# Kernel tuning notes

Hardware: AMD Instinct MI355X
Metric: run time of the kernel (lower is better)

## Reference

```python
import jax, jax.numpy as jnp
import numpy as np

N_IN, N_HID, N_OUT = 128, 1024, 64
B, T = 128, 256
SIGMA_NEU = 0.05
ALPHA = 0.25

def setup_inputs() -> dict:
    key = jax.random.key(0)
    ks = jax.random.split(key, 6)
    input_signal = jax.random.normal(ks[0], (B, T, N_IN), dtype=jnp.float32)
    hidden = jax.random.normal(ks[1], (B, N_HID), dtype=jnp.float32)
    w_in_w = jax.random.normal(ks[2], (N_HID, N_IN), dtype=jnp.float32) / np.sqrt(N_IN)
    w_hh_w = jax.random.normal(ks[3], (N_HID, N_HID), dtype=jnp.float32) / np.sqrt(N_HID)
    w_hh_b = jnp.zeros((N_HID,), dtype=jnp.float32)
    w_out_w = jax.random.normal(ks[4], (N_OUT, N_HID), dtype=jnp.float32) / np.sqrt(N_HID)
    alpha = jnp.full((N_HID,), ALPHA, dtype=jnp.float32)
    noise_raw = jax.random.normal(ks[5], (B, N_HID), dtype=jnp.float32)
    return {
        'input_signal': input_signal,
        'hidden': hidden,
        'w_in_w': w_in_w,
        'w_hh_w': w_hh_w,
        'w_hh_b': w_hh_b,
        'w_out_w': w_out_w,
        'alpha': alpha,
        'noise_raw': noise_raw,
        'perturbation_timing': 100,
    }

def reference(input_signal, hidden, w_in_w, w_hh_w, w_hh_b, w_out_w, alpha, noise_raw, perturbation_timing):
    # input_signal: [B, T, n_in] -> time-major [T, B, n_in]
    x = jnp.swapaxes(input_signal, 0, 1)
    length = x.shape[0]
    # neural noise injected only at t == perturbation_timing (torch: randn*sigma*sqrt(alpha))
    noise = noise_raw * SIGMA_NEU * jnp.sqrt(alpha)

    def step(h, inp):
        t, x_t = inp
        activated = jnp.tanh(h)
        tmp = x_t @ w_in_w.T + activated @ w_hh_w.T + w_hh_b  # [B, n_hid]
        h_new = (1.0 - alpha) * h + alpha * tmp
        h_new = jnp.where(t == perturbation_timing, h_new + noise, h_new)
        out = h_new @ w_out_w.T  # [B, n_out]
        return h_new, (h_new, out)

    h_final, (hs, outs) = jax.lax.scan(step, hidden, (jnp.arange(length), x))
    hidden_list = jnp.swapaxes(hs, 0, 1)   # [B, T, n_hid]
    output_list = jnp.swapaxes(outs, 0, 1)  # [B, T, n_out]
    return hidden_list, output_list, h_final
```

## Files before the change

kernel.cpp:

```cpp
#include <hip/hip_runtime.h>

typedef _Float16 half8 __attribute__((ext_vector_type(8)));
typedef float floatx4 __attribute__((ext_vector_type(4)));
typedef float floatx2 __attribute__((ext_vector_type(2)));

#define N_IN   128
#define N_HID  1024
#define N_OUT  64
#define BB     128
#define TT     256

#define WHH_STRIDE 1032
#define WIN_STRIDE 136
#define RED_STRIDE 33

__device__ __forceinline__ float tanh_fast(float v) {
    float e = __expf(2.0f * v);
    return 1.0f - 2.0f / (e + 1.0f);
}

__global__ __launch_bounds__(256, 1) void rnn_seq_kernel(
    const float* __restrict__ x,
    const float* __restrict__ h0,
    const float* __restrict__ w_in,
    const float* __restrict__ w_hh,
    const float* __restrict__ w_hh_b,
    const float* __restrict__ alpha,
    const float* __restrict__ noise_raw,
    const int* __restrict__ pt_ptr,
    float* __restrict__ out,
    _Float16* __restrict__ actbuf,
    unsigned int* __restrict__ flags)
{
    __shared__ _Float16 Whh_hi[32 * WHH_STRIDE];
    __shared__ _Float16 Whh_lo[32 * WHH_STRIDE];
    __shared__ _Float16 Win_hi[32 * WIN_STRIDE];
    __shared__ _Float16 Win_lo[32 * WIN_STRIDE];
    __shared__ float red[4 * 16 * RED_STRIDE];

    const int tid  = threadIdx.x;
    const int bid  = blockIdx.x;
    const int g    = bid & 7;
    const int s    = bid >> 3;
    const int w    = tid >> 6;
    const int lane = tid & 63;
    const int quad = lane >> 4;
    const int mrow = lane & 15;

    for (int p = 0; p < 32; ++p) {
        int f4 = tid + (p << 8);
        int c  = f4 >> 8;
        int k4 = (f4 & 255) << 2;
        floatx4 wv = *(const floatx4*)(w_hh + ((size_t)(s * 32 + c) << 10) + k4);
        #pragma unroll
        for (int i = 0; i < 4; ++i) {
            float v = wv[i];
            _Float16 hi = (_Float16)v;
            _Float16 lo = (_Float16)((v - (float)hi) * 1024.0f);
            Whh_hi[c * WHH_STRIDE + k4 + i] = hi;
            Whh_lo[c * WHH_STRIDE + k4 + i] = lo;
        }
    }
    for (int p = 0; p < 4; ++p) {
        int f4 = tid + (p << 8);
        int c  = f4 >> 5;
        int k4 = (f4 & 31) << 2;
        floatx4 wv = *(const floatx4*)(w_in + ((size_t)(s * 32 + c) << 7) + k4);
        #pragma unroll
        for (int i = 0; i < 4; ++i) {
            float v = wv[i];
            _Float16 hi = (_Float16)v;
            _Float16 lo = (_Float16)((v - (float)hi) * 1024.0f);
            Win_hi[c * WIN_STRIDE + k4 + i] = hi;
            Win_lo[c * WIN_STRIDE + k4 + i] = lo;
        }
    }
    __syncthreads();

    half8 bh0[8], bl0[8], bh1[8], bl1[8];
    #pragma unroll
    for (int kc = 0; kc < 8; ++kc) {
        int kb = (w << 8) + (kc << 5) + (quad << 3);
        bh0[kc] = *(const half8*)&Whh_hi[mrow * WHH_STRIDE + kb];
        bl0[kc] = *(const half8*)&Whh_lo[mrow * WHH_STRIDE + kb];
        bh1[kc] = *(const half8*)&Whh_hi[(16 + mrow) * WHH_STRIDE + kb];
        bl1[kc] = *(const half8*)&Whh_lo[(16 + mrow) * WHH_STRIDE + kb];
    }
    half8 wi_h0, wi_l0, wi_h1, wi_l1;
    {
        int kb = (w << 5) + (quad << 3);
        wi_h0 = *(const half8*)&Win_hi[mrow * WIN_STRIDE + kb];
        wi_l0 = *(const half8*)&Win_lo[mrow * WIN_STRIDE + kb];
        wi_h1 = *(const half8*)&Win_hi[(16 + mrow) * WIN_STRIDE + kb];
        wi_l1 = *(const half8*)&Win_lo[(16 + mrow) * WIN_STRIDE + kb];
    }

    const int r   = tid >> 4;
    const int c2  = tid & 15;
    const int b   = g * 16 + r;
    const int j0  = s * 32 + 2 * c2;
    const floatx2 a2  = *(const floatx2*)&alpha[j0];
    const floatx2 bi2 = *(const floatx2*)&w_hh_b[j0];
    const floatx2 nr2 = *(const floatx2*)&noise_raw[((size_t)b << 10) + j0];
    const float n0 = nr2.x * 0.05f * __builtin_sqrtf(a2.x);
    const float n1 = nr2.y * 0.05f * __builtin_sqrtf(a2.y);
    const int pt = *pt_ptr;
    floatx2 h2 = *(const floatx2*)&h0[((size_t)b << 10) + j0];
    float hA = h2.x, hB = h2.y;

    {
        unsigned int* act1_32 = (unsigned int*)(actbuf + BB * N_HID);
        union { _Float16 h[2]; unsigned int u; } pk;
        pk.h[0] = (_Float16)tanh_fast(hA);
        pk.h[1] = (_Float16)tanh_fast(hB);
        __hip_atomic_store(&act1_32[(((unsigned)b << 10) + j0) >> 1], pk.u,
                           __ATOMIC_RELAXED, __HIP_MEMORY_SCOPE_AGENT);
    }
    __syncthreads();
    if (tid == 0)
        __hip_atomic_store(&flags[((unsigned)g) * 32u + s], 1u,
                           __ATOMIC_RELAXED, __HIP_MEMORY_SCOPE_AGENT);

    float* hidden_list = out;
    float* h_final = out + (size_t)BB * TT * N_HID + (size_t)BB * TT * N_OUT;
    const int arow = g * 16 + mrow;

    for (int t = 0; t < TT; ++t) {
        {
            const unsigned tok = (unsigned)t + 1u;
            const unsigned fidx = ((unsigned)t * 8u + g) * 32u + (w << 3) + (lane & 7);
            while (true) {
                unsigned v = __hip_atomic_load(&flags[fidx], __ATOMIC_RELAXED,
                                               __HIP_MEMORY_SCOPE_AGENT);
                if (__ballot(v == tok) == ~0ull) break;
                __builtin_amdgcn_s_sleep(1);
            }
        }

        half8 afr[8];
        {
            const unsigned long long* actq = (const unsigned long long*)
                (actbuf + (size_t)((t & 1) ^ 1) * (BB * N_HID));
            const unsigned long long* p =
                actq + ((((size_t)arow << 10) + (w << 8) + (quad << 3)) >> 2);
            #pragma unroll
            for (int kc = 0; kc < 8; ++kc) {
                union { unsigned long long u[2]; half8 h; } cv;
                cv.u[0] = __hip_atomic_load(p + kc * 8,     __ATOMIC_RELAXED,
                                            __HIP_MEMORY_SCOPE_AGENT);
                cv.u[1] = __hip_atomic_load(p + kc * 8 + 1, __ATOMIC_RELAXED,
                                            __HIP_MEMORY_SCOPE_AGENT);
                afr[kc] = cv.h;
            }
        }
        half8 xfr;
        {
            const float* xp = x + (((size_t)arow << 8) + t) * N_IN + (w << 5) + (quad << 3);
            floatx4 x0 = *(const floatx4*)xp;
            floatx4 x1 = *(const floatx4*)(xp + 4);
            #pragma unroll
            for (int i = 0; i < 4; ++i) { xfr[i] = (_Float16)x0[i]; xfr[4 + i] = (_Float16)x1[i]; }
        }

        floatx4 acch0 = {0.f,0.f,0.f,0.f}, acch1 = {0.f,0.f,0.f,0.f};
        floatx4 accl0 = {0.f,0.f,0.f,0.f}, accl1 = {0.f,0.f,0.f,0.f};

        acch0 = __builtin_amdgcn_mfma_f32_16x16x32_f16(xfr, wi_h0, acch0, 0, 0, 0);
        accl0 = __builtin_amdgcn_mfma_f32_16x16x32_f16(xfr, wi_l0, accl0, 0, 0, 0);
        acch1 = __builtin_amdgcn_mfma_f32_16x16x32_f16(xfr, wi_h1, acch1, 0, 0, 0);
        accl1 = __builtin_amdgcn_mfma_f32_16x16x32_f16(xfr, wi_l1, accl1, 0, 0, 0);

        #pragma unroll
        for (int kc = 0; kc < 8; ++kc) {
            acch0 = __builtin_amdgcn_mfma_f32_16x16x32_f16(afr[kc], bh0[kc], acch0, 0, 0, 0);
            accl0 = __builtin_amdgcn_mfma_f32_16x16x32_f16(afr[kc], bl0[kc], accl0, 0, 0, 0);
            acch1 = __builtin_amdgcn_mfma_f32_16x16x32_f16(afr[kc], bh1[kc], acch1, 0, 0, 0);
            accl1 = __builtin_amdgcn_mfma_f32_16x16x32_f16(afr[kc], bl1[kc], accl1, 0, 0, 0);
        }

        #pragma unroll
        for (int rr = 0; rr < 4; ++rr) {
            red[(w * 16 + quad * 4 + rr) * RED_STRIDE + mrow]
                = acch0[rr] + accl0[rr] * (1.0f / 1024.0f);
            red[(w * 16 + quad * 4 + rr) * RED_STRIDE + 16 + mrow]
                = acch1[rr] + accl1[rr] * (1.0f / 1024.0f);
        }
        __syncthreads();

        float t0v = bi2.x, t1v = bi2.y;
        #pragma unroll
        for (int ww = 0; ww < 4; ++ww) {
            t0v += red[(ww * 16 + r) * RED_STRIDE + 2 * c2];
            t1v += red[(ww * 16 + r) * RED_STRIDE + 2 * c2 + 1];
        }
        hA = (1.0f - a2.x) * hA + a2.x * t0v;
        hB = (1.0f - a2.y) * hB + a2.y * t1v;
        if (t == pt) { hA += n0; hB += n1; }

        floatx2 hv = {hA, hB};
        *(floatx2*)&hidden_list[(((size_t)b << 8) + t) * N_HID + j0] = hv;

        {
            union { _Float16 h[2]; unsigned int u; } pk;
            pk.h[0] = (_Float16)tanh_fast(hA);
            pk.h[1] = (_Float16)tanh_fast(hB);
            unsigned int* actw32 = (unsigned int*)(actbuf + (size_t)(t & 1) * (BB * N_HID));
            __hip_atomic_store(&actw32[(((unsigned)b << 10) + j0) >> 1], pk.u,
                               __ATOMIC_RELAXED, __HIP_MEMORY_SCOPE_AGENT);
        }

        __syncthreads();
        if (tid == 0)
            __hip_atomic_store(&flags[((unsigned)(t + 1) * 8u + g) * 32u + s],
                               (unsigned)t + 2u,
                               __ATOMIC_RELAXED, __HIP_MEMORY_SCOPE_AGENT);
    }

    *(floatx2*)&h_final[((size_t)b << 10) + j0] = (floatx2){hA, hB};
}

__global__ __launch_bounds__(256) void out_gemm_kernel(
    const float* __restrict__ hl,
    const float* __restrict__ w_out,
    float* __restrict__ outp)
{
    __shared__ _Float16 Wb[64 * 264];
    const int tid  = threadIdx.x;
    const int w    = tid >> 6;
    const int lane = tid & 63;
    const int quad = lane >> 4;
    const int mrow = lane & 15;
    const size_t rowbase = (size_t)blockIdx.x << 6;

    floatx4 acc0 = {0.f,0.f,0.f,0.f}, acc1 = {0.f,0.f,0.f,0.f};
    floatx4 acc2 = {0.f,0.f,0.f,0.f}, acc3 = {0.f,0.f,0.f,0.f};

    for (int kc = 0; kc < 4; ++kc) {
        __syncthreads();
        for (int p = 0; p < 16; ++p) {
            int f4 = tid + (p << 8);
            int n  = f4 >> 6;
            int k4 = (f4 & 63) << 2;
            floatx4 wv = *(const floatx4*)(w_out + ((size_t)n << 10) + (kc << 8) + k4);
            #pragma unroll
            for (int i = 0; i < 4; ++i) Wb[n * 264 + k4 + i] = (_Float16)wv[i];
        }
        __syncthreads();
        for (int kk = 0; kk < 8; ++kk) {
            const float* ap = hl + (rowbase + (w << 4) + mrow) * 1024
                                 + (kc << 8) + (kk << 5) + (quad << 3);
            floatx4 a0v = *(const floatx4*)ap;
            floatx4 a1v = *(const floatx4*)(ap + 4);
            half8 afr;
            #pragma unroll
            for (int i = 0; i < 4; ++i) { afr[i] = (_Float16)a0v[i]; afr[4 + i] = (_Float16)a1v[i]; }
            int kb = (kk << 5) + (quad << 3);
            half8 bf0 = *(const half8*)&Wb[(mrow)      * 264 + kb];
            half8 bf1 = *(const half8*)&Wb[(16 + mrow) * 264 + kb];
            half8 bf2 = *(const half8*)&Wb[(32 + mrow) * 264 + kb];
            half8 bf3 = *(const half8*)&Wb[(48 + mrow) * 264 + kb];
            acc0 = __builtin_amdgcn_mfma_f32_16x16x32_f16(afr, bf0, acc0, 0, 0, 0);
            acc1 = __builtin_amdgcn_mfma_f32_16x16x32_f16(afr, bf1, acc1, 0, 0, 0);
            acc2 = __builtin_amdgcn_mfma_f32_16x16x32_f16(afr, bf2, acc2, 0, 0, 0);
            acc3 = __builtin_amdgcn_mfma_f32_16x16x32_f16(afr, bf3, acc3, 0, 0, 0);
        }
    }
    size_t rb = rowbase + (w << 4);
    #pragma unroll
    for (int rr = 0; rr < 4; ++rr) {
        outp[(rb + quad * 4 + rr) * 64 +      mrow] = acc0[rr];
        outp[(rb + quad * 4 + rr) * 64 + 16 + mrow] = acc1[rr];
        outp[(rb + quad * 4 + rr) * 64 + 32 + mrow] = acc2[rr];
        outp[(rb + quad * 4 + rr) * 64 + 48 + mrow] = acc3[rr];
    }
}

extern "C" void kernel_launch(void* const* d_in, const int* in_sizes, int n_in,
                              void* d_out, int out_size, void* d_ws, size_t ws_size,
                              hipStream_t stream)
{
    const float* x      = (const float*)d_in[0];
    const float* h0     = (const float*)d_in[1];
    const float* w_in   = (const float*)d_in[2];
    const float* w_hh   = (const float*)d_in[3];
    const float* w_hh_b = (const float*)d_in[4];
    const float* w_out  = (const float*)d_in[5];
    const float* alpha  = (const float*)d_in[6];
    const float* noise  = (const float*)d_in[7];
    const int*   pt     = (const int*)d_in[8];
    float* out = (float*)d_out;

    _Float16* actbuf = (_Float16*)d_ws;
    unsigned int* flags =
        (unsigned int*)((char*)d_ws + (size_t)2 * BB * N_HID * sizeof(_Float16));

    hipLaunchKernelGGL(rnn_seq_kernel, dim3(256), dim3(256), 0, stream,
                       x, h0, w_in, w_hh, w_hh_b, alpha, noise, pt, out, actbuf, flags);

    float* output_list = out + (size_t)BB * TT * N_HID;
    hipLaunchKernelGGL(out_gemm_kernel, dim3(512), dim3(256), 0, stream,
                       out, w_out, output_list);
}
```

Before: 1.203 ms.

## Fuse output projection into recurrent kernel using fp16 hidden-state exchange buffer

Drops the separate output GEMM kernel. Each block now computes its two output columns per timestep with one lagged MFMA chain over an fp16 copy of the previous hidden state. That copy is exchanged through a new double-buffered workspace alongside the tanh activations. The change also prefetches x before the flag spin-wait, removes the s_sleep from the spin loop, and moves the hidden_list store after the flag release. It adds a second global store and load of the full hidden state per step, plus a final extra wait and GEMM after the loop.

```diff
diff --git a/kernel.cpp b/kernel.cpp
--- a/kernel.cpp
+++ b/kernel.cpp
@@ -25,11 +25,13 @@
     const float* __restrict__ w_in,
     const float* __restrict__ w_hh,
     const float* __restrict__ w_hh_b,
+    const float* __restrict__ w_out,
     const float* __restrict__ alpha,
     const float* __restrict__ noise_raw,
     const int* __restrict__ pt_ptr,
     float* __restrict__ out,
     _Float16* __restrict__ actbuf,
+    _Float16* __restrict__ hbuf,
     unsigned int* __restrict__ flags)
 {
     __shared__ _Float16 Whh_hi[32 * WHH_STRIDE];
@@ -37,6 +39,7 @@
     __shared__ _Float16 Win_hi[32 * WIN_STRIDE];
     __shared__ _Float16 Win_lo[32 * WIN_STRIDE];
     __shared__ float red[4 * 16 * RED_STRIDE];
+    __shared__ float red2[4 * 16 * 2];
 
     const int tid  = threadIdx.x;
     const int bid  = blockIdx.x;
@@ -93,6 +96,24 @@
         wi_l0 = *(const half8*)&Win_lo[mrow * WIN_STRIDE + kb];
         wi_h1 = *(const half8*)&Win_hi[(16 + mrow) * WIN_STRIDE + kb];
         wi_l1 = *(const half8*)&Win_lo[(16 + mrow) * WIN_STRIDE + kb];
+    }
+
+    half8 wo[8];
+    if (mrow < 2) {
+        const float* wp = w_out + ((size_t)(s * 2 + mrow) << 10) + (w << 8) + (quad << 3);
+        #pragma unroll
+        for (int kc = 0; kc < 8; ++kc) {
+            floatx4 a0 = *(const floatx4*)(wp + (kc << 5));
+            floatx4 a1 = *(const floatx4*)(wp + (kc << 5) + 4);
+            #pragma unroll
+            for (int i = 0; i < 4; ++i) { wo[kc][i] = (_Float16)a0[i]; wo[kc][4 + i] = (_Float16)a1[i]; }
+        }
+    } else {
+        #pragma unroll
+        for (int kc = 0; kc < 8; ++kc) {
+            #pragma unroll
+            for (int i = 0; i < 8; ++i) wo[kc][i] = (_Float16)0.0f;
+        }
     }
 
     const int r   = tid >> 4;
@@ -110,11 +131,15 @@
 
     {
         unsigned int* act1_32 = (unsigned int*)(actbuf + BB * N_HID);
-        union { _Float16 h[2]; unsigned int u; } pk;
-        pk.h[0] = (_Float16)tanh_fast(hA);
-        pk.h[1] = (_Float16)tanh_fast(hB);
-        __hip_atomic_store(&act1_32[(((unsigned)b << 10) + j0) >> 1], pk.u,
-                           __ATOMIC_RELAXED, __HIP_MEMORY_SCOPE_AGENT);
+        unsigned int* h1_32   = (unsigned int*)(hbuf   + BB * N_HID);
+        union { _Float16 h[2]; unsigned int u; } pk, pk2;
+        pk.h[0]  = (_Float16)tanh_fast(hA);
+        pk.h[1]  = (_Float16)tanh_fast(hB);
+        pk2.h[0] = (_Float16)hA;
+        pk2.h[1] = (_Float16)hB;
+        const unsigned idx = (((unsigned)b << 10) + j0) >> 1;
+        __hip_atomic_store(&act1_32[idx], pk.u,  __ATOMIC_RELAXED, __HIP_MEMORY_SCOPE_AGENT);
+        __hip_atomic_store(&h1_32[idx],   pk2.u, __ATOMIC_RELAXED, __HIP_MEMORY_SCOPE_AGENT);
     }
     __syncthreads();
     if (tid == 0)
@@ -122,10 +147,15 @@
                            __ATOMIC_RELAXED, __HIP_MEMORY_SCOPE_AGENT);
 
     float* hidden_list = out;
+    float* output_list = out + (size_t)BB * TT * N_HID;
     float* h_final = out + (size_t)BB * TT * N_HID + (size_t)BB * TT * N_OUT;
     const int arow = g * 16 + mrow;
 
     for (int t = 0; t < TT; ++t) {
+        const float* xp = x + (((size_t)arow << 8) + t) * N_IN + (w << 5) + (quad << 3);
+        floatx4 xf0 = *(const floatx4*)xp;
+        floatx4 xf1 = *(const floatx4*)(xp + 4);
+
         {
             const unsigned tok = (unsigned)t + 1u;
             const unsigned fidx = ((unsigned)t * 8u + g) * 32u + (w << 3) + (lane & 7);
@@ -133,7 +163,6 @@
                 unsigned v = __hip_atomic_load(&flags[fidx], __ATOMIC_RELAXED,
                                                __HIP_MEMORY_SCOPE_AGENT);
                 if (__ballot(v == tok) == ~0ull) break;
-                __builtin_amdgcn_s_sleep(1);
             }
         }
 
@@ -153,14 +182,25 @@
                 afr[kc] = cv.h;
             }
         }
+        half8 hfr[8];
+        {
+            const unsigned long long* hq = (const unsigned long long*)
+                (hbuf + (size_t)((t & 1) ^ 1) * (BB * N_HID));
+            const unsigned long long* p =
+                hq + ((((size_t)arow << 10) + (w << 8) + (quad << 3)) >> 2);
+            #pragma unroll
+            for (int kc = 0; kc < 8; ++kc) {
+                union { unsigned long long u[2]; half8 h; } cv;
+                cv.u[0] = __hip_atomic_load(p + kc * 8,     __ATOMIC_RELAXED,
+                                            __HIP_MEMORY_SCOPE_AGENT);
+                cv.u[1] = __hip_atomic_load(p + kc * 8 + 1, __ATOMIC_RELAXED,
+                                            __HIP_MEMORY_SCOPE_AGENT);
+                hfr[kc] = cv.h;
+            }
+        }
         half8 xfr;
-        {
-            const float* xp = x + (((size_t)arow << 8) + t) * N_IN + (w << 5) + (quad << 3);
-            floatx4 x0 = *(const floatx4*)xp;
-            floatx4 x1 = *(const floatx4*)(xp + 4);
-            #pragma unroll
-            for (int i = 0; i < 4; ++i) { xfr[i] = (_Float16)x0[i]; xfr[4 + i] = (_Float16)x1[i]; }
-        }
+        #pragma unroll
+        for (int i = 0; i < 4; ++i) { xfr[i] = (_Float16)xf0[i]; xfr[4 + i] = (_Float16)xf1[i]; }
 
         floatx4 acch0 = {0.f,0.f,0.f,0.f}, acch1 = {0.f,0.f,0.f,0.f};
         floatx4 accl0 = {0.f,0.f,0.f,0.f}, accl1 = {0.f,0.f,0.f,0.f};
@@ -178,6 +218,11 @@
             accl1 = __builtin_amdgcn_mfma_f32_16x16x32_f16(afr[kc], bl1[kc], accl1, 0, 0, 0);
         }
 
+        floatx4 aco = {0.f,0.f,0.f,0.f};
+        #pragma unroll
+        for (int kc = 0; kc < 8; ++kc)
+            aco = __builtin_amdgcn_mfma_f32_16x16x32_f16(hfr[kc], wo[kc], aco, 0, 0, 0);
+
         #pragma unroll
         for (int rr = 0; rr < 4; ++rr) {
             red[(w * 16 + quad * 4 + rr) * RED_STRIDE + mrow]
@@ -185,6 +230,11 @@
             red[(w * 16 + quad * 4 + rr) * RED_STRIDE + 16 + mrow]
                 = acch1[rr] + accl1[rr] * (1.0f / 1024.0f);
         }
+        if (mrow < 2) {
+            #pragma unroll
+            for (int rr = 0; rr < 4; ++rr)
+                red2[(w * 16 + quad * 4 + rr) * 2 + mrow] = aco[rr];
+        }
         __syncthreads();
 
         float t0v = bi2.x, t1v = bi2.y;
@@ -193,20 +243,28 @@
             t0v += red[(ww * 16 + r) * RED_STRIDE + 2 * c2];
             t1v += red[(ww * 16 + r) * RED_STRIDE + 2 * c2 + 1];
         }
+        if (t > 0 && tid < 32) {
+            int rr_ = tid >> 1, oc2 = tid & 1;
+            float v = red2[(rr_) * 2 + oc2] + red2[(16 + rr_) * 2 + oc2]
+                    + red2[(32 + rr_) * 2 + oc2] + red2[(48 + rr_) * 2 + oc2];
+            output_list[((size_t)(g * 16 + rr_) * TT + (t - 1)) * 64 + s * 2 + oc2] = v;
+        }
+
         hA = (1.0f - a2.x) * hA + a2.x * t0v;
         hB = (1.0f - a2.y) * hB + a2.y * t1v;
         if (t == pt) { hA += n0; hB += n1; }
 
-        floatx2 hv = {hA, hB};
-        *(floatx2*)&hidden_list[(((size_t)b << 8) + t) * N_HID + j0] = hv;
-
         {
-            union { _Float16 h[2]; unsigned int u; } pk;
-            pk.h[0] = (_Float16)tanh_fast(hA);
-            pk.h[1] = (_Float16)tanh_fast(hB);
+            union { _Float16 h[2]; unsigned int u; } pk, pk2;
+            pk.h[0]  = (_Float16)tanh_fast(hA);
+            pk.h[1]  = (_Float16)tanh_fast(hB);
+            pk2.h[0] = (_Float16)hA;
+            pk2.h[1] = (_Float16)hB;
             unsigned int* actw32 = (unsigned int*)(actbuf + (size_t)(t & 1) * (BB * N_HID));
-            __hip_atomic_store(&actw32[(((unsigned)b << 10) + j0) >> 1], pk.u,
-                               __ATOMIC_RELAXED, __HIP_MEMORY_SCOPE_AGENT);
+            unsigned int* hw32   = (unsigned int*)(hbuf   + (size_t)(t & 1) * (BB * N_HID));
+            const unsigned idx = (((unsigned)b << 10) + j0) >> 1;
+            __hip_atomic_store(&actw32[idx], pk.u,  __ATOMIC_RELAXED, __HIP_MEMORY_SCOPE_AGENT);
+            __hip_atomic_store(&hw32[idx],   pk2.u, __ATOMIC_RELAXED, __HIP_MEMORY_SCOPE_AGENT);
         }
 
         __syncthreads();
@@ -214,64 +272,53 @@
             __hip_atomic_store(&flags[((unsigned)(t + 1) * 8u + g) * 32u + s],
                                (unsigned)t + 2u,
                                __ATOMIC_RELAXED, __HIP_MEMORY_SCOPE_AGENT);
+
+        floatx2 hv = {hA, hB};
+        *(floatx2*)&hidden_list[(((size_t)b << 8) + t) * N_HID + j0] = hv;
     }
 
     *(floatx2*)&h_final[((size_t)b << 10) + j0] = (floatx2){hA, hB};
-}
-
-__global__ __launch_bounds__(256) void out_gemm_kernel(
-    const float* __restrict__ hl,
-    const float* __restrict__ w_out,
-    float* __restrict__ outp)
-{
-    __shared__ _Float16 Wb[64 * 264];
-    const int tid  = threadIdx.x;
-    const int w    = tid >> 6;
-    const int lane = tid & 63;
-    const int quad = lane >> 4;
-    const int mrow = lane & 15;
-    const size_t rowbase = (size_t)blockIdx.x << 6;
-
-    floatx4 acc0 = {0.f,0.f,0.f,0.f}, acc1 = {0.f,0.f,0.f,0.f};
-    floatx4 acc2 = {0.f,0.f,0.f,0.f}, acc3 = {0.f,0.f,0.f,0.f};
-
-    for (int kc = 0; kc < 4; ++kc) {
+
+    {
+        const unsigned tok = (unsigned)TT + 1u;
+        const unsigned fidx = ((unsigned)TT * 8u + g) * 32u + (w << 3) + (lane & 7);
+        while (true) {
+            unsigned v = __hip_atomic_load(&flags[fidx], __ATOMIC_RELAXED,
+                                           __HIP_MEMORY_SCOPE_AGENT);
+            if (__ballot(v == tok) == ~0ull) break;
+        }
+    }
+    {
+        half8 hfr[8];
+        const unsigned long long* hq = (const unsigned long long*)
+            (hbuf + (size_t)((TT & 1) ^ 1) * (BB * N_HID));
+        const unsigned long long* p =
+            hq + ((((size_t)arow << 10) + (w << 8) + (quad << 3)) >> 2);
+        #pragma unroll
+        for (int kc = 0; kc < 8; ++kc) {
+            union { unsigned long long u[2]; half8 h; } cv;
+            cv.u[0] = __hip_atomic_load(p + kc * 8,     __ATOMIC_RELAXED,
+                                        __HIP_MEMORY_SCOPE_AGENT);
+            cv.u[1] = __hip_atomic_load(p + kc * 8 + 1, __ATOMIC_RELAXED,
+                                        __HIP_MEMORY_SCOPE_AGENT);
+            hfr[kc] = cv.h;
+        }
+        floatx4 aco = {0.f,0.f,0.f,0.f};
+        #pragma unroll
+        for (int kc = 0; kc < 8; ++kc)
+            aco = __builtin_amdgcn_mfma_f32_16x16x32_f16(hfr[kc], wo[kc], aco, 0, 0, 0);
+        if (mrow < 2) {
+            #pragma unroll
+            for (int rr = 0; rr < 4; ++rr)
+                red2[(w * 16 + quad * 4 + rr) * 2 + mrow] = aco[rr];
+        }
         __syncthreads();
-        for (int p = 0; p < 16; ++p) {
-            int f4 = tid + (p << 8);
-            int n  = f4 >> 6;
-            int k4 = (f4 & 63) << 2;
-            floatx4 wv = *(const floatx4*)(w_out + ((size_t)n << 10) + (kc << 8) + k4);
-            #pragma unroll
-            for (int i = 0; i < 4; ++i) Wb[n * 264 + k4 + i] = (_Float16)wv[i];
-        }
-        __syncthreads();
-        for (int kk = 0; kk < 8; ++kk) {
-            const float* ap = hl + (rowbase + (w << 4) + mrow) * 1024
-                                 + (kc << 8) + (kk << 5) + (quad << 3);
-            floatx4 a0v = *(const floatx4*)ap;
-            floatx4 a1v = *(const floatx4*)(ap + 4);
-            half8 afr;
-            #pragma unroll
-            for (int i = 0; i < 4; ++i) { afr[i] = (_Float16)a0v[i]; afr[4 + i] = (_Float16)a1v[i]; }
-            int kb = (kk << 5) + (quad << 3);
-            half8 bf0 = *(const half8*)&Wb[(mrow)      * 264 + kb];
-            half8 bf1 = *(const half8*)&Wb[(16 + mrow) * 264 + kb];
-            half8 bf2 = *(const half8*)&Wb[(32 + mrow) * 264 + kb];
-            half8 bf3 = *(const half8*)&Wb[(48 + mrow) * 264 + kb];
-            acc0 = __builtin_amdgcn_mfma_f32_16x16x32_f16(afr, bf0, acc0, 0, 0, 0);
-            acc1 = __builtin_amdgcn_mfma_f32_16x16x32_f16(afr, bf1, acc1, 0, 0, 0);
-            acc2 = __builtin_amdgcn_mfma_f32_16x16x32_f16(afr, bf2, acc2, 0, 0, 0);
-            acc3 = __builtin_amdgcn_mfma_f32_16x16x32_f16(afr, bf3, acc3, 0, 0, 0);
-        }
-    }
-    size_t rb = rowbase + (w << 4);
-    #pragma unroll
-    for (int rr = 0; rr < 4; ++rr) {
-        outp[(rb + quad * 4 + rr) * 64 +      mrow] = acc0[rr];
-        outp[(rb + quad * 4 + rr) * 64 + 16 + mrow] = acc1[rr];
-        outp[(rb + quad * 4 + rr) * 64 + 32 + mrow] = acc2[rr];
-        outp[(rb + quad * 4 + rr) * 64 + 48 + mrow] = acc3[rr];
+        if (tid < 32) {
+            int rr_ = tid >> 1, oc2 = tid & 1;
+            float v = red2[(rr_) * 2 + oc2] + red2[(16 + rr_) * 2 + oc2]
+                    + red2[(32 + rr_) * 2 + oc2] + red2[(48 + rr_) * 2 + oc2];
+            output_list[((size_t)(g * 16 + rr_) * TT + (TT - 1)) * 64 + s * 2 + oc2] = v;
+        }
     }
 }
 
@@ -291,13 +338,11 @@
     float* out = (float*)d_out;
 
     _Float16* actbuf = (_Float16*)d_ws;
+    _Float16* hbuf   = actbuf + (size_t)2 * BB * N_HID;
     unsigned int* flags =
-        (unsigned int*)((char*)d_ws + (size_t)2 * BB * N_HID * sizeof(_Float16));
+        (unsigned int*)((char*)d_ws + (size_t)4 * BB * N_HID * sizeof(_Float16));
 
     hipLaunchKernelGGL(rnn_seq_kernel, dim3(256), dim3(256), 0, stream,
-                       x, h0, w_in, w_hh, w_hh_b, alpha, noise, pt, out, actbuf, flags);
-
-    float* output_list = out + (size_t)BB * TT * N_HID;
-    hipLaunchKernelGGL(out_gemm_kernel, dim3(512), dim3(256), 0, stream,
-                       out, w_out, output_list);
+                       x, h0, w_in, w_hh, w_hh_b, w_out, alpha, noise, pt, out,
+                       actbuf, hbuf, flags);
 }
```

Measured after the change: 1.459 ms. +21.2%, slower.

## Fuse output projection into recurrent kernel via per-step MFMA and atomic accumulation

Applied to the files above, without the earlier changes.

Removes the separate output GEMM kernel. Each block now computes its 32-column slice of h_t @ W_out^T with one MFMA per wave per step and accumulates into output_list with float atomicAdd, after zeroing its region at start. It also moves the hidden_list store to after the flag release, prefetches x before the spin-wait, and drops s_sleep from the polling loop. The cost is 32-way atomic contention on every output element and extra per-step work on the serial critical path, in exchange for removing the second launch and the full reread of hidden_list.

```diff
diff --git a/kernel.cpp b/kernel.cpp
--- a/kernel.cpp
+++ b/kernel.cpp
@@ -13,6 +13,7 @@
 #define WHH_STRIDE 1032
 #define WIN_STRIDE 136
 #define RED_STRIDE 33
+#define HSH_STRIDE 40
 
 __device__ __forceinline__ float tanh_fast(float v) {
     float e = __expf(2.0f * v);
@@ -25,6 +26,7 @@
     const float* __restrict__ w_in,
     const float* __restrict__ w_hh,
     const float* __restrict__ w_hh_b,
+    const float* __restrict__ w_out,
     const float* __restrict__ alpha,
     const float* __restrict__ noise_raw,
     const int* __restrict__ pt_ptr,
@@ -37,6 +39,7 @@
     __shared__ _Float16 Win_hi[32 * WIN_STRIDE];
     __shared__ _Float16 Win_lo[32 * WIN_STRIDE];
     __shared__ float red[4 * 16 * RED_STRIDE];
+    __shared__ _Float16 hsh[16 * HSH_STRIDE];
 
     const int tid  = threadIdx.x;
     const int bid  = blockIdx.x;
@@ -93,6 +96,15 @@
         wi_l0 = *(const half8*)&Win_lo[mrow * WIN_STRIDE + kb];
         wi_h1 = *(const half8*)&Win_hi[(16 + mrow) * WIN_STRIDE + kb];
         wi_l1 = *(const half8*)&Win_lo[(16 + mrow) * WIN_STRIDE + kb];
+    }
+
+    half8 wo;
+    {
+        const float* wp = w_out + ((size_t)((w << 4) + mrow) << 10) + (s << 5) + (quad << 3);
+        floatx4 a0 = *(const floatx4*)wp;
+        floatx4 a1 = *(const floatx4*)(wp + 4);
+        #pragma unroll
+        for (int i = 0; i < 4; ++i) { wo[i] = (_Float16)a0[i]; wo[4 + i] = (_Float16)a1[i]; }
     }
 
     const int r   = tid >> 4;
@@ -108,6 +120,10 @@
     floatx2 h2 = *(const floatx2*)&h0[((size_t)b << 10) + j0];
     float hA = h2.x, hB = h2.y;
 
+    float* hidden_list = out;
+    float* output_list = out + (size_t)BB * TT * N_HID;
+    float* h_final = out + (size_t)BB * TT * N_HID + (size_t)BB * TT * N_OUT;
+
     {
         unsigned int* act1_32 = (unsigned int*)(actbuf + BB * N_HID);
         union { _Float16 h[2]; unsigned int u; } pk;
@@ -115,17 +131,26 @@
         pk.h[1] = (_Float16)tanh_fast(hB);
         __hip_atomic_store(&act1_32[(((unsigned)b << 10) + j0) >> 1], pk.u,
                            __ATOMIC_RELAXED, __HIP_MEMORY_SCOPE_AGENT);
+
+        unsigned long long* zb = (unsigned long long*)
+            (output_list + ((size_t)b * TT + (s << 3)) * 64 + (c2 << 5));
+        #pragma unroll
+        for (int i = 0; i < 16; ++i)
+            __hip_atomic_store(zb + i, 0ull, __ATOMIC_RELAXED,
+                               __HIP_MEMORY_SCOPE_AGENT);
     }
     __syncthreads();
     if (tid == 0)
         __hip_atomic_store(&flags[((unsigned)g) * 32u + s], 1u,
                            __ATOMIC_RELAXED, __HIP_MEMORY_SCOPE_AGENT);
 
-    float* hidden_list = out;
-    float* h_final = out + (size_t)BB * TT * N_HID + (size_t)BB * TT * N_OUT;
     const int arow = g * 16 + mrow;
 
     for (int t = 0; t < TT; ++t) {
+        const float* xp = x + (((size_t)arow << 8) + t) * N_IN + (w << 5) + (quad << 3);
+        floatx4 xf0 = *(const floatx4*)xp;
+        floatx4 xf1 = *(const floatx4*)(xp + 4);
+
         {
             const unsigned tok = (unsigned)t + 1u;
             const unsigned fidx = ((unsigned)t * 8u + g) * 32u + (w << 3) + (lane & 7);
@@ -133,7 +158,6 @@
                 unsigned v = __hip_atomic_load(&flags[fidx], __ATOMIC_RELAXED,
                                                __HIP_MEMORY_SCOPE_AGENT);
                 if (__ballot(v == tok) == ~0ull) break;
-                __builtin_amdgcn_s_sleep(1);
             }
         }
 
@@ -154,13 +178,8 @@
             }
         }
         half8 xfr;
-        {
-            const float* xp = x + (((size_t)arow << 8) + t) * N_IN + (w << 5) + (quad << 3);
-            floatx4 x0 = *(const floatx4*)xp;
-            floatx4 x1 = *(const floatx4*)(xp + 4);
-            #pragma unroll
-            for (int i = 0; i < 4; ++i) { xfr[i] = (_Float16)x0[i]; xfr[4 + i] = (_Float16)x1[i]; }
-        }
+        #pragma unroll
+        for (int i = 0; i < 4; ++i) { xfr[i] = (_Float16)xf0[i]; xfr[4 + i] = (_Float16)xf1[i]; }
 
         floatx4 acch0 = {0.f,0.f,0.f,0.f}, acch1 = {0.f,0.f,0.f,0.f};
         floatx4 accl0 = {0.f,0.f,0.f,0.f}, accl1 = {0.f,0.f,0.f,0.f};
@@ -197,16 +216,16 @@
         hB = (1.0f - a2.y) * hB + a2.y * t1v;
         if (t == pt) { hA += n0; hB += n1; }
 
-        floatx2 hv = {hA, hB};
-        *(floatx2*)&hidden_list[(((size_t)b << 8) + t) * N_HID + j0] = hv;
-
-        {
-            union { _Float16 h[2]; unsigned int u; } pk;
-            pk.h[0] = (_Float16)tanh_fast(hA);
-            pk.h[1] = (_Float16)tanh_fast(hB);
+        {
+            union { _Float16 h[2]; unsigned int u; } pk, pk2;
+            pk.h[0]  = (_Float16)tanh_fast(hA);
+            pk.h[1]  = (_Float16)tanh_fast(hB);
             unsigned int* actw32 = (unsigned int*)(actbuf + (size_t)(t & 1) * (BB * N_HID));
             __hip_atomic_store(&actw32[(((unsigned)b << 10) + j0) >> 1], pk.u,
                                __ATOMIC_RELAXED, __HIP_MEMORY_SCOPE_AGENT);
+            pk2.h[0] = (_Float16)hA;
+            pk2.h[1] = (_Float16)hB;
+            ((unsigned int*)hsh)[r * (HSH_STRIDE / 2) + c2] = pk2.u;
         }
 
         __syncthreads();
@@ -214,65 +233,23 @@
             __hip_atomic_store(&flags[((unsigned)(t + 1) * 8u + g) * 32u + s],
                                (unsigned)t + 2u,
                                __ATOMIC_RELAXED, __HIP_MEMORY_SCOPE_AGENT);
+
+
+        floatx2 hv = {hA, hB};
+        *(floatx2*)&hidden_list[(((size_t)b << 8) + t) * N_HID + j0] = hv;
+
+        {
+            half8 ha = *(const half8*)&hsh[mrow * HSH_STRIDE + (quad << 3)];
+            floatx4 aco = {0.f,0.f,0.f,0.f};
+            aco = __builtin_amdgcn_mfma_f32_16x16x32_f16(ha, wo, aco, 0, 0, 0);
+            #pragma unroll
+            for (int rr = 0; rr < 4; ++rr)
+                atomicAdd(&output_list[((size_t)(g * 16 + quad * 4 + rr) * TT + t) * 64
+                                       + (w << 4) + mrow], aco[rr]);
+        }
     }
 
     *(floatx2*)&h_final[((size_t)b << 10) + j0] = (floatx2){hA, hB};
-}
-
-__global__ __launch_bounds__(256) void out_gemm_kernel(
-    const float* __restrict__ hl,
-    const float* __restrict__ w_out,
-    float* __restrict__ outp)
-{
-    __shared__ _Float16 Wb[64 * 264];
-    const int tid  = threadIdx.x;
-    const int w    = tid >> 6;
-    const int lane = tid & 63;
-    const int quad = lane >> 4;
-    const int mrow = lane & 15;
-    const size_t rowbase = (size_t)blockIdx.x << 6;
-
-    floatx4 acc0 = {0.f,0.f,0.f,0.f}, acc1 = {0.f,0.f,0.f,0.f};
-    floatx4 acc2 = {0.f,0.f,0.f,0.f}, acc3 = {0.f,0.f,0.f,0.f};
-
-    for (int kc = 0; kc < 4; ++kc) {
-        __syncthreads();
-        for (int p = 0; p < 16; ++p) {
-            int f4 = tid + (p << 8);
-            int n  = f4 >> 6;
-            int k4 = (f4 & 63) << 2;
-            floatx4 wv = *(const floatx4*)(w_out + ((size_t)n << 10) + (kc << 8) + k4);
-            #pragma unroll
-            for (int i = 0; i < 4; ++i) Wb[n * 264 + k4 + i] = (_Float16)wv[i];
-        }
-        __syncthreads();
-        for (int kk = 0; kk < 8; ++kk) {
-            const float* ap = hl + (rowbase + (w << 4) + mrow) * 1024
-                                 + (kc << 8) + (kk << 5) + (quad << 3);
-            floatx4 a0v = *(const floatx4*)ap;
-            floatx4 a1v = *(const floatx4*)(ap + 4);
-            half8 afr;
-            #pragma unroll
-            for (int i = 0; i < 4; ++i) { afr[i] = (_Float16)a0v[i]; afr[4 + i] = (_Float16)a1v[i]; }
-            int kb = (kk << 5) + (quad << 3);
-            half8 bf0 = *(const half8*)&Wb[(mrow)      * 264 + kb];
-            half8 bf1 = *(const half8*)&Wb[(16 + mrow) * 264 + kb];
-            half8 bf2 = *(const half8*)&Wb[(32 + mrow) * 264 + kb];
-            half8 bf3 = *(const half8*)&Wb[(48 + mrow) * 264 + kb];
-            acc0 = __builtin_amdgcn_mfma_f32_16x16x32_f16(afr, bf0, acc0, 0, 0, 0);
-            acc1 = __builtin_amdgcn_mfma_f32_16x16x32_f16(afr, bf1, acc1, 0, 0, 0);
-            acc2 = __builtin_amdgcn_mfma_f32_16x16x32_f16(afr, bf2, acc2, 0, 0, 0);
-            acc3 = __builtin_amdgcn_mfma_f32_16x16x32_f16(afr, bf3, acc3, 0, 0, 0);
-        }
-    }
-    size_t rb = rowbase + (w << 4);
-    #pragma unroll
-    for (int rr = 0; rr < 4; ++rr) {
-        outp[(rb + quad * 4 + rr) * 64 +      mrow] = acc0[rr];
-        outp[(rb + quad * 4 + rr) * 64 + 16 + mrow] = acc1[rr];
-        outp[(rb + quad * 4 + rr) * 64 + 32 + mrow] = acc2[rr];
-        outp[(rb + quad * 4 + rr) * 64 + 48 + mrow] = acc3[rr];
-    }
 }
 
 extern "C" void kernel_launch(void* const* d_in, const int* in_sizes, int n_in,
@@ -295,9 +272,6 @@
         (unsigned int*)((char*)d_ws + (size_t)2 * BB * N_HID * sizeof(_Float16));
 
     hipLaunchKernelGGL(rnn_seq_kernel, dim3(256), dim3(256), 0, stream,
-                       x, h0, w_in, w_hh, w_hh_b, alpha, noise, pt, out, actbuf, flags);
-
-    float* output_list = out + (size_t)BB * TT * N_HID;
-    hipLaunchKernelGGL(out_gemm_kernel, dim3(512), dim3(256), 0, stream,
-                       out, w_out, output_list);
+                       x, h0, w_in, w_hh, w_hh_b, w_out, alpha, noise, pt, out,
+                       actbuf, flags);
 }
```

Measured after the change: 1.123 ms. -6.7%, faster.
